# Kernel optimization log

Measured on AMD Instinct MI355X. Metric: run time of the kernel, lower is better.

The kernel has to match this reference:

```python
import jax, jax.numpy as jnp
import numpy as np

NUM_HEADS = 12
QUAD_C = 5.0

def setup_inputs() -> dict:
    key = jax.random.key(0)
    k1, k2, k3 = jax.random.split(key, 3)
    B, N, C = 8, 1024, 768
    x = jax.random.normal(k1, (B, N, C), dtype=jnp.float32)
    qkv_w = jax.random.normal(k2, (3 * C, C), dtype=jnp.float32) * (C ** -0.5)
    proj_w = jax.random.normal(k3, (C, C), dtype=jnp.float32) * (C ** -0.5)
    proj_b = jnp.zeros((C,), dtype=jnp.float32)
    return {"x": x, "qkv_w": qkv_w, "proj_w": proj_w, "proj_b": proj_b}

def reference(x, qkv_w, proj_w, proj_b):
    B, N, C = x.shape
    H = NUM_HEADS
    hd = C // H
    scale = hd ** -0.5
    # qkv projection: [B,N,3C] -> [3,B,H,N,hd]
    qkv = (x @ qkv_w.T).reshape(B, N, 3, H, hd).transpose(2, 0, 3, 1, 4)
    q, k, v = qkv[0], qkv[1], qkv[2]
    # explicit N x N attention scores
    attn = jnp.einsum('bhnd,bhmd->bhnm', q, k) * scale
    # Quad2 normalization: square(x + c) / row-sum
    t = jnp.square(attn + QUAD_C)
    attn = t / jnp.sum(t, axis=-1, keepdims=True)
    out = jnp.einsum('bhnm,bhmd->bhnd', attn, v)  # [B,H,N,hd]
    out = out.transpose(0, 2, 1, 3).reshape(B, N, C)
    return out @ proj_w.T + proj_b
```

## Files before the change

kernel.cpp:

```cpp
#include <hip/hip_runtime.h>
#include <hip/hip_bf16.h>
#include <stdint.h>


typedef short  s8v  __attribute__((ext_vector_type(8)));
typedef float  f4v  __attribute__((ext_vector_type(4)));

__device__ inline uint16_t f2bf(float f) {
    union { float f; uint32_t u; } c; c.f = f;
    uint32_t u = c.u;
    u += 0x7fffu + ((u >> 16) & 1u);
    return (uint16_t)(u >> 16);
}
__device__ inline uint32_t pack2bf(float a, float b) {
    union { __hip_bfloat162 v; uint32_t u; } c;
    c.v = __float22bfloat162_rn(float2{a, b});
    return c.u;
}

__device__ inline void cp16(const uint16_t* g, uint16_t* l) {
    __builtin_amdgcn_global_load_lds(
        (const __attribute__((address_space(1))) void*)g,
        (__attribute__((address_space(3))) void*)l, 16, 0, 0);
}

__global__ __launch_bounds__(256) void cvt_all(
    const float* __restrict__ x, const float* __restrict__ qw,
    const float* __restrict__ pw, uint16_t* __restrict__ dst)
{
    int i = blockIdx.x * 256 + threadIdx.x;
    if (i >= 1081344) return;
    const float* s;
    if (i < 786432)       s = x  + (size_t)i * 8;
    else if (i < 1007616) s = qw + ((size_t)i - 786432) * 8;
    else                  s = pw + ((size_t)i - 1007616) * 8;
    const float4* sp = reinterpret_cast<const float4*>(s);
    float4 a = sp[0], b = sp[1];
    s8v o;
    o[0] = (short)f2bf(a.x); o[1] = (short)f2bf(a.y);
    o[2] = (short)f2bf(a.z); o[3] = (short)f2bf(a.w);
    o[4] = (short)f2bf(b.x); o[5] = (short)f2bf(b.y);
    o[6] = (short)f2bf(b.z); o[7] = (short)f2bf(b.w);
    *reinterpret_cast<s8v*>(dst + (size_t)i * 8) = o;
}

template <int EPI>
__global__ __launch_bounds__(512, 2) void gemm_pipe(
    const uint16_t* __restrict__ A, const uint16_t* __restrict__ Bm,
    uint16_t* __restrict__ qb, uint16_t* __restrict__ kb, uint16_t* __restrict__ vb,
    const float* __restrict__ bias, float* __restrict__ Cout, int K, int GN)
{
    __shared__ uint16_t Al[3][128 * 64];
    __shared__ uint16_t Bl[3][256 * 64];

    const int tid  = threadIdx.x;
    const int wave = tid >> 6, lane = tid & 63;
    const int quad = lane >> 4, l16 = lane & 15;
    const int wM = wave >> 2, wN = wave & 3;

    const int nwg = (int)gridDim.x;
    const int wg  = ((int)blockIdx.x & 7) * (nwg >> 3) + ((int)blockIdx.x >> 3);
    const int bM = wg / GN, bN = wg - bM * GN;

    const uint16_t* Ag = A  + (size_t)bM * 128 * K;
    const uint16_t* Bg = Bm + (size_t)bN * 256 * K;

    f4v acc[4][4];
#pragma unroll
    for (int i = 0; i < 4; i++)
#pragma unroll
        for (int j = 0; j < 4; j++) { f4v z = {0.f, 0.f, 0.f, 0.f}; acc[i][j] = z; }

    const int nt = K >> 6;

    auto stage = [&](int t, int slot) {
        const int kc = t << 6;
        uint16_t* as = &Al[slot][0];
        uint16_t* bs = &Bl[slot][0];
#pragma unroll
        for (int u = 0; u < 2; ++u) {
            const int ch = tid + u * 512;
            const int r  = ch >> 3, lc = (ch & 7) ^ (r & 7);
            cp16(Ag + (size_t)r * K + kc + lc * 8, as + ch * 8);
        }
#pragma unroll
        for (int u = 0; u < 4; ++u) {
            const int ch = tid + u * 512;
            const int r  = ch >> 3, lc = (ch & 7) ^ (r & 7);
            cp16(Bg + (size_t)r * K + kc + lc * 8, bs + ch * 8);
        }
    };

    auto compute = [&](int slot) {
        const uint16_t* as = &Al[slot][0];
        const uint16_t* bs = &Bl[slot][0];
        s8v af[4][2], bfr[4][2];
#pragma unroll
        for (int x = 0; x < 4; ++x) {
            const int ra = wM * 64 + x * 16 + l16;
            const int rb = wN * 64 + x * 16 + l16;
#pragma unroll
            for (int kk = 0; kk < 2; ++kk) {
                const int pa = (kk * 4 + quad) ^ (ra & 7);
                const int pb = (kk * 4 + quad) ^ (rb & 7);
                af[x][kk]  = *reinterpret_cast<const s8v*>(as + ra * 64 + pa * 8);
                bfr[x][kk] = *reinterpret_cast<const s8v*>(bs + rb * 64 + pb * 8);
            }
        }
        __builtin_amdgcn_s_setprio(1);
#pragma unroll
        for (int kk = 0; kk < 2; ++kk)
#pragma unroll
            for (int tm = 0; tm < 4; ++tm)
#pragma unroll
                for (int tn = 0; tn < 4; ++tn)
                    acc[tm][tn] = __builtin_amdgcn_mfma_f32_16x16x32_bf16(
                        af[tm][kk], bfr[tn][kk], acc[tm][tn], 0, 0, 0);
        __builtin_amdgcn_s_setprio(0);
    };

    stage(0, 0);
    stage(1, 1);

    int cs = 0;
    for (int t = 0; t < nt - 1; ++t) {
        asm volatile("s_waitcnt vmcnt(6)" ::: "memory");
        __builtin_amdgcn_s_barrier();
        if (t + 2 < nt) {
            int ss = cs + 2; if (ss >= 3) ss -= 3;
            stage(t + 2, ss);
        }
        compute(cs);
        cs = (cs == 2) ? 0 : cs + 1;
    }
    asm volatile("s_waitcnt vmcnt(0)" ::: "memory");
    __builtin_amdgcn_s_barrier();
    compute(cs);

#pragma unroll
    for (int tm = 0; tm < 4; tm++) {
#pragma unroll
        for (int tn = 0; tn < 4; tn++) {
            const int col = bN * 256 + wN * 64 + tn * 16 + l16;
            if (EPI == 0) {
                const int three = col / 768;
                const int rem   = col - three * 768;
                const int h = rem >> 6, d = rem & 63;
                const int n0 = bM * 128 + wM * 64 + tm * 16 + quad * 4;
                const int b = n0 >> 10, n = n0 & 1023;
                if (three == 2) {
                    ushort4 pk;
                    pk.x = f2bf(acc[tm][tn][0]);
                    pk.y = f2bf(acc[tm][tn][1]);
                    pk.z = f2bf(acc[tm][tn][2]);
                    pk.w = f2bf(acc[tm][tn][3]);
                    *reinterpret_cast<ushort4*>(
                        &vb[((size_t)((b * 12 + h) * 64 + d)) * 1024 + n]) = pk;
                } else {
                    uint16_t* dst = (three == 0) ? qb : kb;
#pragma unroll
                    for (int reg = 0; reg < 4; reg++)
                        dst[((size_t)((b * 12 + h) * 1024 + n + reg)) * 64 + d] =
                            f2bf(acc[tm][tn][reg]);
                }
            } else {
#pragma unroll
                for (int reg = 0; reg < 4; reg++) {
                    const int row = bM * 128 + wM * 64 + tm * 16 + quad * 4 + reg;
                    Cout[(size_t)row * 768 + col] = acc[tm][tn][reg] + bias[col];
                }
            }
        }
    }
}

__global__ __launch_bounds__(128, 2) void attn_quad(
    const uint16_t* __restrict__ Q, const uint16_t* __restrict__ K,
    const uint16_t* __restrict__ VT, uint16_t* __restrict__ O)
{
    const int qt = blockIdx.x;
    const int bh = blockIdx.y;
    const int b = bh / 12, h = bh - (bh / 12) * 12;
    const uint16_t* Qp = Q  + (size_t)bh * 65536;
    const uint16_t* Kp = K  + (size_t)bh * 65536;
    const uint16_t* Vp = VT + (size_t)bh * 65536;

    const int tid  = threadIdx.x;
    const int wave = tid >> 6, lane = tid & 63;
    const int quad = lane >> 4, l16 = lane & 15;

    __shared__ uint16_t Kl[64 * 64];
    __shared__ uint16_t Vl[64 * 64];
    __shared__ uint16_t Pl[2][16][80];

    s8v qf[4][2];
#pragma unroll
    for (int s = 0; s < 4; s++) {
        const uint16_t* qp = Qp + (size_t)(qt * 128 + wave * 64 + s * 16 + l16) * 64 + quad * 8;
        qf[s][0] = *reinterpret_cast<const s8v*>(qp);
        qf[s][1] = *reinterpret_cast<const s8v*>(qp + 32);
    }

    s8v ones;
#pragma unroll
    for (int i = 0; i < 8; i++) ones[i] = (short)0x3F80;

    f4v U[4][4], U5[4];
#pragma unroll
    for (int s = 0; s < 4; s++) {
        f4v z = {0.f, 0.f, 0.f, 0.f};
        U5[s] = z;
#pragma unroll
        for (int c = 0; c < 4; c++) U[s][c] = z;
    }

    for (int mt = 0; mt < 16; mt++) {
        __syncthreads();
#pragma unroll
        for (int r = 0; r < 4; r++) {
            const int e   = (tid + r * 128) * 8;
            const int row = e >> 6;
            const int cl  = ((e >> 3) & 7) ^ (row & 7);
            cp16(Kp + (size_t)mt * 4096 + (size_t)row * 64 + cl * 8, &Kl[e]);
            cp16(Vp + (size_t)row * 1024 + mt * 64 + cl * 8, &Vl[e]);
        }
        __syncthreads();

        s8v kf[4][2], vf[4][2];
#pragma unroll
        for (int c = 0; c < 4; c++) {
            const int rr = c * 16 + l16;
#pragma unroll
            for (int kk = 0; kk < 2; kk++) {
                const int pc = (kk * 4 + quad) ^ (rr & 7);
                kf[c][kk] = *reinterpret_cast<const s8v*>(&Kl[rr * 64 + (pc << 3)]);
                vf[c][kk] = *reinterpret_cast<const s8v*>(&Vl[rr * 64 + (pc << 3)]);
            }
        }

#pragma unroll
        for (int s = 0; s < 4; s++) {
            f4v st[4];
#pragma unroll
            for (int cm = 0; cm < 4; cm++) {
                f4v z = {0.f, 0.f, 0.f, 0.f};
                z = __builtin_amdgcn_mfma_f32_16x16x32_bf16(kf[cm][0], qf[s][0], z, 0, 0, 0);
                z = __builtin_amdgcn_mfma_f32_16x16x32_bf16(kf[cm][1], qf[s][1], z, 0, 0, 0);
                st[cm] = z;
            }
#pragma unroll
            for (int cm = 0; cm < 4; cm++) {
                float t0 = st[cm][0] * 0.125f + 5.0f; t0 *= t0;
                float t1 = st[cm][1] * 0.125f + 5.0f; t1 *= t1;
                float t2 = st[cm][2] * 0.125f + 5.0f; t2 *= t2;
                float t3 = st[cm][3] * 0.125f + 5.0f; t3 *= t3;
                uint2 pk; pk.x = pack2bf(t0, t1); pk.y = pack2bf(t2, t3);
                *reinterpret_cast<uint2*>(&Pl[wave][l16][cm * 16 + quad * 4]) = pk;
            }
#pragma unroll
            for (int kc = 0; kc < 2; kc++) {
                s8v pf = *reinterpret_cast<const s8v*>(&Pl[wave][l16][kc * 32 + quad * 8]);
                U5[s] = __builtin_amdgcn_mfma_f32_16x16x32_bf16(pf, ones, U5[s], 0, 0, 0);
#pragma unroll
                for (int cd = 0; cd < 4; cd++)
                    U[s][cd] = __builtin_amdgcn_mfma_f32_16x16x32_bf16(pf, vf[cd][kc], U[s][cd], 0, 0, 0);
            }
        }
    }

#pragma unroll
    for (int s = 0; s < 4; s++) {
        float inv[4];
#pragma unroll
        for (int reg = 0; reg < 4; reg++) inv[reg] = 1.0f / U5[s][reg];
#pragma unroll
        for (int cd = 0; cd < 4; cd++) {
#pragma unroll
            for (int reg = 0; reg < 4; reg++) {
                const int n = qt * 128 + wave * 64 + s * 16 + quad * 4 + reg;
                const int d = cd * 16 + l16;
                O[((size_t)(b * 1024 + n)) * 768 + h * 64 + d] = f2bf(U[s][cd][reg] * inv[reg]);
            }
        }
    }
}

extern "C" void kernel_launch(void* const* d_in, const int* in_sizes, int n_in,
                              void* d_out, int out_size, void* d_ws, size_t ws_size,
                              hipStream_t stream)
{
    const float* x      = (const float*)d_in[0];
    const float* qkv_w  = (const float*)d_in[1];
    const float* proj_w = (const float*)d_in[2];
    const float* proj_b = (const float*)d_in[3];
    float* out = (float*)d_out;

    const size_t NEL = (size_t)8 * 1024 * 768;
    uint16_t* xb  = (uint16_t*)d_ws;
    uint16_t* qwb = xb  + NEL;
    uint16_t* pwb = qwb + 1769472;
    uint16_t* qb  = pwb + 589824;
    uint16_t* kb  = qb  + NEL;
    uint16_t* vb  = kb  + NEL;
    uint16_t* ao  = vb  + NEL;

    cvt_all<<<4224, 256, 0, stream>>>(x, qkv_w, proj_w, xb);

    gemm_pipe<0><<<576, 512, 0, stream>>>(xb, qwb, qb, kb, vb, nullptr, nullptr, 768, 9);
    attn_quad<<<dim3(8, 96), 128, 0, stream>>>(qb, kb, vb, ao);
    gemm_pipe<1><<<192, 512, 0, stream>>>(ao, pwb, nullptr, nullptr, nullptr, proj_b, out, 768, 3);
}
```

Baseline: 202.6 us.

## Split GEMM K-tile into two phases interleaving LDS reads, prefetch and MFMA

Restructures the GEMM main loop so each 64-wide K tile is processed in two 32-wide halves. Each half loads its fragments, issues part of the next-next tile's global-to-LDS copies, then runs its MFMAs under a barrier. K also becomes a compile-time constant so loops and addresses can be fully specialised. The aim is to spread global loads across the loop and shrink fragment register use, at the cost of extra barriers per tile.

```diff
diff --git a/kernel.cpp b/kernel.cpp
--- a/kernel.cpp
+++ b/kernel.cpp
@@ -45,11 +45,14 @@
 }
 
 template <int EPI>
-__global__ __launch_bounds__(512, 2) void gemm_pipe(
+__global__ __launch_bounds__(512, 2) void gemm_8ph(
     const uint16_t* __restrict__ A, const uint16_t* __restrict__ Bm,
     uint16_t* __restrict__ qb, uint16_t* __restrict__ kb, uint16_t* __restrict__ vb,
-    const float* __restrict__ bias, float* __restrict__ Cout, int K, int GN)
+    const float* __restrict__ bias, float* __restrict__ Cout, int GN)
 {
+    constexpr int K  = 768;
+    constexpr int NT = K / 64;
+
     __shared__ uint16_t Al[3][128 * 64];
     __shared__ uint16_t Bl[3][256 * 64];
 
@@ -71,71 +74,85 @@
 #pragma unroll
         for (int j = 0; j < 4; j++) { f4v z = {0.f, 0.f, 0.f, 0.f}; acc[i][j] = z; }
 
-    const int nt = K >> 6;
-
-    auto stage = [&](int t, int slot) {
-        const int kc = t << 6;
-        uint16_t* as = &Al[slot][0];
-        uint16_t* bs = &Bl[slot][0];
-#pragma unroll
-        for (int u = 0; u < 2; ++u) {
-            const int ch = tid + u * 512;
-            const int r  = ch >> 3, lc = (ch & 7) ^ (r & 7);
-            cp16(Ag + (size_t)r * K + kc + lc * 8, as + ch * 8);
-        }
-#pragma unroll
-        for (int u = 0; u < 4; ++u) {
-            const int ch = tid + u * 512;
-            const int r  = ch >> 3, lc = (ch & 7) ^ (r & 7);
-            cp16(Bg + (size_t)r * K + kc + lc * 8, bs + ch * 8);
-        }
+    auto stA = [&](int t, int slot, int u) {
+        const int ch = tid + u * 512;
+        const int r  = ch >> 3, lc = (ch & 7) ^ (r & 7);
+        cp16(Ag + (size_t)r * K + t * 64 + lc * 8, &Al[slot][ch * 8]);
     };
-
-    auto compute = [&](int slot) {
+    auto stB = [&](int t, int slot, int u) {
+        const int ch = tid + u * 512;
+        const int r  = ch >> 3, lc = (ch & 7) ^ (r & 7);
+        cp16(Bg + (size_t)r * K + t * 64 + lc * 8, &Bl[slot][ch * 8]);
+    };
+
+    stA(0, 0, 0); stA(0, 0, 1);
+    stB(0, 0, 0); stB(0, 0, 1); stB(0, 0, 2); stB(0, 0, 3);
+    stA(1, 1, 0); stA(1, 1, 1);
+    stB(1, 1, 0); stB(1, 1, 1); stB(1, 1, 2); stB(1, 1, 3);
+    asm volatile("s_waitcnt vmcnt(6)" ::: "memory");
+    __builtin_amdgcn_s_barrier();
+
+    int slot = 0;
+    for (int g = 0; g < NT; ++g) {
+        int ss = slot + 2; if (ss >= 3) ss -= 3;
+        const bool pf = (g + 2 < NT);
         const uint16_t* as = &Al[slot][0];
         const uint16_t* bs = &Bl[slot][0];
-        s8v af[4][2], bfr[4][2];
+
+        s8v af[4], bq[4];
 #pragma unroll
         for (int x = 0; x < 4; ++x) {
             const int ra = wM * 64 + x * 16 + l16;
+            const int pa = quad ^ (ra & 7);
+            af[x] = *reinterpret_cast<const s8v*>(as + ra * 64 + pa * 8);
+        }
+#pragma unroll
+        for (int x = 0; x < 4; ++x) {
             const int rb = wN * 64 + x * 16 + l16;
-#pragma unroll
-            for (int kk = 0; kk < 2; ++kk) {
-                const int pa = (kk * 4 + quad) ^ (ra & 7);
-                const int pb = (kk * 4 + quad) ^ (rb & 7);
-                af[x][kk]  = *reinterpret_cast<const s8v*>(as + ra * 64 + pa * 8);
-                bfr[x][kk] = *reinterpret_cast<const s8v*>(bs + rb * 64 + pb * 8);
-            }
-        }
+            const int pb = quad ^ (rb & 7);
+            bq[x] = *reinterpret_cast<const s8v*>(bs + rb * 64 + pb * 8);
+        }
+        if (pf) { stA(g + 2, ss, 0); stA(g + 2, ss, 1); stB(g + 2, ss, 0); }
+        __builtin_amdgcn_s_barrier();
         __builtin_amdgcn_s_setprio(1);
 #pragma unroll
-        for (int kk = 0; kk < 2; ++kk)
-#pragma unroll
-            for (int tm = 0; tm < 4; ++tm)
-#pragma unroll
-                for (int tn = 0; tn < 4; ++tn)
-                    acc[tm][tn] = __builtin_amdgcn_mfma_f32_16x16x32_bf16(
-                        af[tm][kk], bfr[tn][kk], acc[tm][tn], 0, 0, 0);
+        for (int tm = 0; tm < 4; ++tm)
+#pragma unroll
+            for (int tn = 0; tn < 4; ++tn)
+                acc[tm][tn] = __builtin_amdgcn_mfma_f32_16x16x32_bf16(
+                    af[tm], bq[tn], acc[tm][tn], 0, 0, 0);
         __builtin_amdgcn_s_setprio(0);
-    };
-
-    stage(0, 0);
-    stage(1, 1);
-
-    int cs = 0;
-    for (int t = 0; t < nt - 1; ++t) {
-        asm volatile("s_waitcnt vmcnt(6)" ::: "memory");
         __builtin_amdgcn_s_barrier();
-        if (t + 2 < nt) {
-            int ss = cs + 2; if (ss >= 3) ss -= 3;
-            stage(t + 2, ss);
-        }
-        compute(cs);
-        cs = (cs == 2) ? 0 : cs + 1;
-    }
-    asm volatile("s_waitcnt vmcnt(0)" ::: "memory");
-    __builtin_amdgcn_s_barrier();
-    compute(cs);
+
+#pragma unroll
+        for (int x = 0; x < 4; ++x) {
+            const int ra = wM * 64 + x * 16 + l16;
+            const int pa = (4 + quad) ^ (ra & 7);
+            af[x] = *reinterpret_cast<const s8v*>(as + ra * 64 + pa * 8);
+        }
+#pragma unroll
+        for (int x = 0; x < 4; ++x) {
+            const int rb = wN * 64 + x * 16 + l16;
+            const int pb = (4 + quad) ^ (rb & 7);
+            bq[x] = *reinterpret_cast<const s8v*>(bs + rb * 64 + pb * 8);
+        }
+        if (pf) { stB(g + 2, ss, 1); stB(g + 2, ss, 2); stB(g + 2, ss, 3); }
+        __builtin_amdgcn_s_barrier();
+        __builtin_amdgcn_s_setprio(1);
+#pragma unroll
+        for (int tm = 0; tm < 4; ++tm)
+#pragma unroll
+            for (int tn = 0; tn < 4; ++tn)
+                acc[tm][tn] = __builtin_amdgcn_mfma_f32_16x16x32_bf16(
+                    af[tm], bq[tn], acc[tm][tn], 0, 0, 0);
+        __builtin_amdgcn_s_setprio(0);
+
+        if (g < NT - 2)       asm volatile("s_waitcnt vmcnt(6)" ::: "memory");
+        else if (g == NT - 2) asm volatile("s_waitcnt vmcnt(0)" ::: "memory");
+        if (g < NT - 1) __builtin_amdgcn_s_barrier();
+
+        slot = (slot == 2) ? 0 : slot + 1;
+    }
 
 #pragma unroll
     for (int tm = 0; tm < 4; tm++) {
@@ -306,7 +323,7 @@
 
     cvt_all<<<4224, 256, 0, stream>>>(x, qkv_w, proj_w, xb);
 
-    gemm_pipe<0><<<576, 512, 0, stream>>>(xb, qwb, qb, kb, vb, nullptr, nullptr, 768, 9);
+    gemm_8ph<0><<<576, 512, 0, stream>>>(xb, qwb, qb, kb, vb, nullptr, nullptr, 9);
     attn_quad<<<dim3(8, 96), 128, 0, stream>>>(qb, kb, vb, ao);
-    gemm_pipe<1><<<192, 512, 0, stream>>>(ao, pwb, nullptr, nullptr, nullptr, proj_b, out, 768, 3);
-}
+    gemm_8ph<1><<<192, 512, 0, stream>>>(ao, pwb, nullptr, nullptr, nullptr, proj_b, out, 3);
+}
```

Result: faster. 197.8 us (-2.4%).
